# Performance work log

Measured on AMD Instinct MI355X. Metric: run time of the kernel, lower is better.

The kernel has to match this reference:

```python
import jax, jax.numpy as jnp
import numpy as np

N_NODES = 10000
N_GRAPHS = 64
NEG_SLOPE = 0.2  # PyG GATConv default


def _glorot(key, shape):
    fan_in, fan_out = shape[0], shape[-1]
    lim = jnp.sqrt(6.0 / (fan_in + fan_out))
    return jax.random.uniform(key, shape, jnp.float32, -lim, lim)


def setup_inputs() -> dict:
    key = jax.random.key(0)
    ks = jax.random.split(key, 12)
    x = jax.random.normal(ks[0], (N_NODES, 128), jnp.float32)
    edge_index = jax.random.randint(ks[1], (2, 160000), 0, N_NODES, jnp.int64)
    batch = jnp.sort(jax.random.randint(ks[2], (N_NODES,), 0, N_GRAPHS, jnp.int64))
    # GATConv 1: 128 -> 512 (heads=1)
    W1 = _glorot(ks[3], (128, 512))
    a_src1 = _glorot(ks[4], (1, 512))[0]
    a_dst1 = _glorot(ks[5], (1, 512))[0]
    b1 = jnp.zeros((512,), jnp.float32)
    # GATConv 2: 512 -> 64
    W2 = _glorot(ks[6], (512, 64))
    a_src2 = _glorot(ks[7], (1, 64))[0]
    a_dst2 = _glorot(ks[8], (1, 64))[0]
    b2 = jnp.zeros((64,), jnp.float32)
    # fc1: 64 -> 2
    fcW = _glorot(ks[9], (64, 2))
    fcb = jnp.zeros((2,), jnp.float32)
    return {"x": x, "edge_index": edge_index, "batch": batch,
            "W1": W1, "a_src1": a_src1, "a_dst1": a_dst1, "b1": b1,
            "W2": W2, "a_src2": a_src2, "a_dst2": a_dst2, "b2": b2,
            "fcW": fcW, "fcb": fcb}


def _gat_conv(x, src, dst, W, a_src, a_dst, b, n_nodes):
    # h: [N, out]; per-edge attention over incoming edges of each dst node
    h = x @ W
    alpha_s = h @ a_src  # [N]
    alpha_d = h @ a_dst  # [N]
    e = jax.nn.leaky_relu(alpha_s[src] + alpha_d[dst], NEG_SLOPE)  # [E]
    e_max = jax.ops.segment_max(e, dst, num_segments=n_nodes)
    ee = jnp.exp(e - e_max[dst])
    denom = jax.ops.segment_sum(ee, dst, num_segments=n_nodes)
    alpha = ee / denom[dst]  # softmax over edges sharing a dst
    out = jax.ops.segment_sum(alpha[:, None] * h[src], dst, num_segments=n_nodes)
    return out + b


def reference(x, edge_index, batch, W1, a_src1, a_dst1, b1,
              W2, a_src2, a_dst2, b2, fcW, fcb):
    n = x.shape[0]
    # add self loops (PyG GATConv default)
    loop = jnp.arange(n, dtype=edge_index.dtype)
    src = jnp.concatenate([edge_index[0], loop])
    dst = jnp.concatenate([edge_index[1], loop])
    h = jax.nn.relu(_gat_conv(x, src, dst, W1, a_src1, a_dst1, b1, n))
    h = jax.nn.relu(_gat_conv(h, src, dst, W2, a_src2, a_dst2, b2, n))
    # global mean pool over graphs
    sums = jax.ops.segment_sum(h, batch, num_segments=N_GRAPHS)
    cnts = jax.ops.segment_sum(jnp.ones((n,), h.dtype), batch, num_segments=N_GRAPHS)
    pooled = sums / jnp.maximum(cnts, 1.0)[:, None]
    # dropout is identity at inference
    return pooled @ fcW + fcb
```

## Files before the change

### kernel.cpp

```cpp
#include <hip/hip_runtime.h>
#include <hip/hip_bf16.h>

#define NEG_SLOPE 0.2f
#define CAP 64

typedef __attribute__((ext_vector_type(8))) short bf16x8;
typedef __attribute__((ext_vector_type(4))) float f32x4;

__device__ __forceinline__ unsigned short f2bf(float f){
  __hip_bfloat16 h = __float2bfloat16(f);
  return *reinterpret_cast<unsigned short*>(&h);
}

__global__ __launch_bounds__(256) void kPre(int N,
    const float* __restrict__ W1, const float* __restrict__ as1v, const float* __restrict__ ad1v,
    const float* __restrict__ W2, const float* __restrict__ as2v, const float* __restrict__ ad2v,
    float* __restrict__ ws1, float* __restrict__ wd1,
    float* __restrict__ ws2, float* __restrict__ wd2,
    unsigned short* __restrict__ W1T, unsigned short* __restrict__ W2T,
    int* __restrict__ cnt){
  const int t = threadIdx.x, blk = blockIdx.x, G = gridDim.x;
  __shared__ unsigned short tile[64][66];

  for (int i = blk * 256 + t; i < N; i += G * 256) cnt[i] = 0;

  if (blk < 160){
    int b = blk * 4 + (t >> 6);
    int l = t & 63;
    float s = 0.f, d = 0.f;
    if (b < 128){
      #pragma unroll
      for (int j = l; j < 512; j += 64){ float w = W1[b * 512 + j]; s += w * as1v[j]; d += w * ad1v[j]; }
    } else {
      int r = b - 128;
      float w = W2[r * 64 + l];
      s = w * as2v[l]; d = w * ad2v[l];
    }
    #pragma unroll
    for (int o = 32; o > 0; o >>= 1){ s += __shfl_xor(s, o); d += __shfl_xor(d, o); }
    if (l == 0){
      if (b < 128){ ws1[b] = s; wd1[b] = d; }
      else        { ws2[b - 128] = s; wd2[b - 128] = d; }
    }
  } else if (blk < 184){
    int u = blk - 160;
    int rr = t >> 6, cl = t & 63;
    if (u < 16){
      int kt = u >> 3, ct = u & 7;
      #pragma unroll
      for (int r = 0; r < 16; ++r){
        int kr = r * 4 + rr;
        tile[kr][cl] = f2bf(W1[(size_t)(kt * 64 + kr) * 512 + ct * 64 + cl]);
      }
      __syncthreads();
      #pragma unroll
      for (int r = 0; r < 16; ++r){
        int cr = r * 4 + rr;
        W1T[(size_t)(ct * 64 + cr) * 128 + kt * 64 + cl] = tile[cl][cr];
      }
    } else {
      int kt = u - 16;
      #pragma unroll
      for (int r = 0; r < 16; ++r){
        int kr = r * 4 + rr;
        tile[kr][cl] = f2bf(W2[(size_t)(kt * 64 + kr) * 64 + cl]);
      }
      __syncthreads();
      #pragma unroll
      for (int r = 0; r < 16; ++r){
        int cr = r * 4 + rr;
        W2T[(size_t)cr * 512 + kt * 64 + cl] = tile[cl][cr];
      }
    }
  }
}

__global__ __launch_bounds__(256) void kScat(const int* __restrict__ ei, int E, int N,
                                             int* __restrict__ cnt, int* __restrict__ csr,
                                             const float* __restrict__ x, const float* __restrict__ ws,
                                             const float* __restrict__ wd,
                                             float* __restrict__ as, float* __restrict__ ad,
                                             int nScat){
  int blk = blockIdx.x;
  if (blk < nScat){
    int i = blk * 256 + threadIdx.x;
    int Etot = E + N;
    if (i >= Etot) return;
    int s, d;
    if (i < E){ s = ei[i]; d = ei[E + i]; } else { s = i - E; d = i - E; }
    int p = atomicAdd(&cnt[d], 1);
    if (p < CAP) csr[(size_t)d * CAP + p] = s;
    return;
  }
  int n = (blk - nScat) * 4 + (threadIdx.x >> 6);
  if (n >= N) return;
  int l = threadIdx.x & 63;
  float2 xv = ((const float2*)(x + (size_t)n * 128))[l];
  float2 sv = ((const float2*)ws)[l];
  float2 dv = ((const float2*)wd)[l];
  float s = xv.x * sv.x + xv.y * sv.y;
  float d = xv.x * dv.x + xv.y * dv.y;
  #pragma unroll
  for (int o = 32; o > 0; o >>= 1){ s += __shfl_xor(s, o); d += __shfl_xor(d, o); }
  if (l == 0){ as[n] = s; ad[n] = d; }
}

template<int F, bool EPI>
__global__ __launch_bounds__(256) void k_aggw(const int* __restrict__ cnt, const int* __restrict__ csr,
    const float* __restrict__ as, const float* __restrict__ ad, const float* __restrict__ h,
    const float* __restrict__ bias, void* __restrict__ out, int N){
  int n = blockIdx.x * 4 + (threadIdx.x >> 6);
  if (n >= N) return;
  int l = threadIdx.x & 63;
  int deg = min(cnt[n], CAP);
  float adv = ad[n];
  int sr0 = 0; float v0 = -3.0e38f;
  if (l < deg){
    sr0 = csr[(size_t)n * CAP + l];
    float vv = as[sr0] + adv;
    v0 = (vv > 0.f) ? vv : NEG_SLOPE * vv;
  }
  float m = v0, ssum = (l < deg) ? 1.f : 0.f;
  #pragma unroll
  for (int o = 32; o > 0; o >>= 1){
    float m2 = __shfl_xor(m, o);
    float s2 = __shfl_xor(ssum, o);
    float mm = fmaxf(m, m2);
    float ns = 0.f;
    if (ssum > 0.f) ns += ssum * __expf(m - mm);
    if (s2  > 0.f) ns += s2  * __expf(m2 - mm);
    m = mm; ssum = ns;
  }
  float inv = 1.0f / ssum;
  float al0 = (l < deg) ? __expf(v0 - m) * inv : 0.f;

  constexpr int EPG = (F == 128) ? 2 : 4;
  constexpr int FL  = (F == 128) ? 32 : 16;
  int p = l / FL;
  int f = l % FL;
  float4 acc = make_float4(0.f, 0.f, 0.f, 0.f);
  int steps = (deg + EPG - 1) / EPG;
  #pragma unroll 4
  for (int i = 0; i < steps; ++i){
    int e = i * EPG + p;
    float a = __shfl(al0, e);
    int s  = __shfl(sr0, e);
    float4 hv = ((const float4*)(h + (size_t)s * F))[f];
    acc.x += a * hv.x; acc.y += a * hv.y; acc.z += a * hv.z; acc.w += a * hv.w;
  }
  if (F == 64){
    acc.x += __shfl_xor(acc.x, 16); acc.y += __shfl_xor(acc.y, 16);
    acc.z += __shfl_xor(acc.z, 16); acc.w += __shfl_xor(acc.w, 16);
  }
  acc.x += __shfl_xor(acc.x, 32); acc.y += __shfl_xor(acc.y, 32);
  acc.z += __shfl_xor(acc.z, 32); acc.w += __shfl_xor(acc.w, 32);
  if (l < FL){
    if (F == 128){
      unsigned short* ob = (unsigned short*)out;
      unsigned int p0 = (unsigned int)f2bf(acc.x) | ((unsigned int)f2bf(acc.y) << 16);
      unsigned int p1 = (unsigned int)f2bf(acc.z) | ((unsigned int)f2bf(acc.w) << 16);
      *(uint2*)(ob + (size_t)n * 128 + f * 4) = make_uint2(p0, p1);
    } else {
      float* ob = (float*)out;
      if (EPI){
        float4 bv = ((const float4*)bias)[f];
        acc.x = fmaxf(acc.x + bv.x, 0.f); acc.y = fmaxf(acc.y + bv.y, 0.f);
        acc.z = fmaxf(acc.z + bv.z, 0.f); acc.w = fmaxf(acc.w + bv.w, 0.f);
      }
      ((float4*)(ob + (size_t)n * F))[f] = acc;
    }
  }
}

#define LROWS 16
__global__ __launch_bounds__(256) void k_layer(
    const unsigned short* __restrict__ xab, const unsigned short* __restrict__ W1T,
    const float* __restrict__ b1,
    const unsigned short* __restrict__ W2T, const float* __restrict__ ws2,
    const float* __restrict__ wd2,
    float* __restrict__ h2, float* __restrict__ as2, float* __restrict__ ad2, int N){
  __shared__ __align__(16) unsigned short xs[16 * 136];
  __shared__ __align__(16) unsigned short gs[16 * 520];
  __shared__ float sred[4][16][2];
  int t = threadIdx.x;
  int w = t >> 6, l = t & 63;
  int lg = l >> 4, ln = l & 15;
  int n0 = blockIdx.x * LROWS;

  {
    int row = t >> 4, seg = t & 15;
    int n = n0 + row; if (n >= N) n = N - 1;
    *(int4*)&xs[row * 136 + seg * 8] = *(const int4*)&xab[(size_t)n * 128 + seg * 8];
  }
  __syncthreads();

  int c0 = w * 128;
  bf16x8 af[4];
  #pragma unroll
  for (int kt = 0; kt < 4; ++kt)
    af[kt] = *reinterpret_cast<const bf16x8*>(&xs[ln * 136 + kt * 32 + lg * 8]);

  f32x4 acc[8];
  #pragma unroll
  for (int nt = 0; nt < 8; ++nt) acc[nt] = (f32x4){0.f, 0.f, 0.f, 0.f};
  #pragma unroll
  for (int nt = 0; nt < 8; ++nt){
    const unsigned short* wp = W1T + (size_t)(c0 + nt * 16 + ln) * 128 + lg * 8;
    #pragma unroll
    for (int kt = 0; kt < 4; ++kt){
      bf16x8 bfr = *reinterpret_cast<const bf16x8*>(wp + kt * 32);
      acc[nt] = __builtin_amdgcn_mfma_f32_16x16x32_bf16(af[kt], bfr, acc[nt], 0, 0, 0);
    }
  }

  float ps4[4] = {0, 0, 0, 0}, pd4[4] = {0, 0, 0, 0};
  #pragma unroll
  for (int nt = 0; nt < 8; ++nt){
    int col = c0 + nt * 16 + ln;
    float bb = b1[col], wsv = ws2[col], wdv = wd2[col];
    #pragma unroll
    for (int r = 0; r < 4; ++r){
      float g = fmaxf(acc[nt][r] + bb, 0.f);
      gs[(lg * 4 + r) * 520 + col] = f2bf(g);
      ps4[r] += g * wsv;
      pd4[r] += g * wdv;
    }
  }
  #pragma unroll
  for (int o = 1; o < 16; o <<= 1){
    #pragma unroll
    for (int r = 0; r < 4; ++r){ ps4[r] += __shfl_xor(ps4[r], o); pd4[r] += __shfl_xor(pd4[r], o); }
  }
  if (ln == 0){
    #pragma unroll
    for (int r = 0; r < 4; ++r){ sred[w][lg * 4 + r][0] = ps4[r]; sred[w][lg * 4 + r][1] = pd4[r]; }
  }
  __syncthreads();
  if (t < 32){
    int r = t >> 1, c = t & 1;
    float v = sred[0][r][c] + sred[1][r][c] + sred[2][r][c] + sred[3][r][c];
    int n = n0 + r;
    if (n < N){ if (c == 0) as2[n] = v; else ad2[n] = v; }
  }

  f32x4 a0 = (f32x4){0.f, 0.f, 0.f, 0.f}, a1 = (f32x4){0.f, 0.f, 0.f, 0.f};
  const unsigned short* wp2 = W2T + (size_t)(w * 16 + ln) * 512 + lg * 8;
  #pragma unroll
  for (int kt = 0; kt < 16; kt += 2){
    bf16x8 afa = *reinterpret_cast<const bf16x8*>(&gs[ln * 520 + kt * 32 + lg * 8]);
    bf16x8 bfa = *reinterpret_cast<const bf16x8*>(wp2 + kt * 32);
    a0 = __builtin_amdgcn_mfma_f32_16x16x32_bf16(afa, bfa, a0, 0, 0, 0);
    bf16x8 afb = *reinterpret_cast<const bf16x8*>(&gs[ln * 520 + (kt + 1) * 32 + lg * 8]);
    bf16x8 bfb = *reinterpret_cast<const bf16x8*>(wp2 + (kt + 1) * 32);
    a1 = __builtin_amdgcn_mfma_f32_16x16x32_bf16(afb, bfb, a1, 0, 0, 0);
  }
  #pragma unroll
  for (int r = 0; r < 4; ++r){
    int n = n0 + lg * 4 + r;
    if (n < N) h2[(size_t)n * 64 + w * 16 + ln] = a0[r] + a1[r];
  }
}

__device__ __forceinline__ int lbound(const int* a, int n, int v){
  int lo = 0, hi = n;
  while (lo < hi){ int mid = (lo + hi) >> 1; if (a[mid] < v) lo = mid + 1; else hi = mid; }
  return lo;
}

__global__ __launch_bounds__(256) void k_poolfc(const float* __restrict__ g2, const int* __restrict__ batch,
                                                const float* __restrict__ fcW, const float* __restrict__ fcb,
                                                float* __restrict__ out, int N){
  int g = blockIdx.x;
  __shared__ int sb[2];
  if (threadIdx.x == 0){ sb[0] = lbound(batch, N, g); sb[1] = lbound(batch, N, g + 1); }
  __syncthreads();
  int r0 = sb[0], r1 = sb[1];
  int f = threadIdx.x & 63, ch = threadIdx.x >> 6;
  float s = 0.f;
  for (int r = r0 + ch; r < r1; r += 4) s += g2[(size_t)r * 64 + f];
  __shared__ float red[4][64];
  red[ch][f] = s;
  __syncthreads();
  if (ch == 0){
    float tot = red[0][f] + red[1][f] + red[2][f] + red[3][f];
    float c = fmaxf((float)(r1 - r0), 1.f);
    float p = tot / c;
    float o0 = p * fcW[f * 2 + 0];
    float o1 = p * fcW[f * 2 + 1];
    #pragma unroll
    for (int o = 32; o > 0; o >>= 1){ o0 += __shfl_xor(o0, o); o1 += __shfl_xor(o1, o); }
    if (f == 0){ out[g * 2 + 0] = o0 + fcb[0]; out[g * 2 + 1] = o1 + fcb[1]; }
  }
}

extern "C" void kernel_launch(void* const* d_in, const int* in_sizes, int n_in,
                              void* d_out, int out_size, void* d_ws, size_t ws_size,
                              hipStream_t stream){
  const float* x    = (const float*)d_in[0];
  const int* ei     = (const int*)d_in[1];
  const int* batch  = (const int*)d_in[2];
  const float* W1   = (const float*)d_in[3];
  const float* as1w = (const float*)d_in[4];
  const float* ad1w = (const float*)d_in[5];
  const float* b1   = (const float*)d_in[6];
  const float* W2   = (const float*)d_in[7];
  const float* as2w = (const float*)d_in[8];
  const float* ad2w = (const float*)d_in[9];
  const float* b2   = (const float*)d_in[10];
  const float* fcW  = (const float*)d_in[11];
  const float* fcb  = (const float*)d_in[12];
  float* out = (float*)d_out;

  const int N    = in_sizes[2];
  const int E    = in_sizes[1] / 2;
  const int NG   = out_size / 2;
  const int Etot = E + N;

  char* base = (char*)d_ws;
  size_t o = 0;
  auto take = [&](size_t bytes) -> char* {
    char* r = base + o;
    o = (o + bytes + 255) & ~(size_t)255;
    return r;
  };
  unsigned short* xa  = (unsigned short*)take((size_t)(N + 16) * 128 * 2);
  float* h2   = (float*)take((size_t)(N + 16) * 64 * 4);
  float* g2   = (float*)take((size_t)(N + 16) * 64 * 4);
  float* as1  = (float*)take((size_t)N * 4);
  float* ad1  = (float*)take((size_t)N * 4);
  float* as2  = (float*)take((size_t)N * 4);
  float* ad2  = (float*)take((size_t)N * 4);
  float* ws1  = (float*)take(128 * 4);
  float* wd1  = (float*)take(128 * 4);
  float* ws2  = (float*)take(512 * 4);
  float* wd2  = (float*)take(512 * 4);
  unsigned short* W1T = (unsigned short*)take((size_t)128 * 512 * 2);
  unsigned short* W2T = (unsigned short*)take((size_t)512 * 64 * 2);
  int*   cnt  = (int*)take((size_t)N * 4);
  int*   csr  = (int*)take((size_t)N * CAP * 4);

  kPre<<<184, 256, 0, stream>>>(N, W1, as1w, ad1w, W2, as2w, ad2w,
                                ws1, wd1, ws2, wd2, W1T, W2T, cnt);

  const int nScat = (Etot + 255) / 256;
  kScat<<<nScat + (N + 3) / 4, 256, 0, stream>>>(ei, E, N, cnt, csr, x, ws1, wd1, as1, ad1, nScat);

  k_aggw<128, false><<<(N + 3) / 4, 256, 0, stream>>>(cnt, csr, as1, ad1, x, b1, (void*)xa, N);
  k_layer<<<(N + LROWS - 1) / LROWS, 256, 0, stream>>>(xa, W1T, b1, W2T, ws2, wd2, h2, as2, ad2, N);
  k_aggw<64, true><<<(N + 3) / 4, 256, 0, stream>>>(cnt, csr, as2, ad2, h2, b2, (void*)g2, N);

  k_poolfc<<<NG, 256, 0, stream>>>(g2, batch, fcW, fcb, out, N);
}
```

Baseline: 82.55 us.

## Fuse layer-1 aggregation into MLP kernel and gather from bf16 copy of x

Layer-1 edge-softmax aggregation now runs inside the layer kernel: each block aggregates its 16 nodes directly into shared memory before the MFMA matmuls. This removes one launch and the global round-trip of the aggregated bf16 features. The gather now reads a bf16 copy of x, made in the prologue kernel, which halves the bytes fetched per neighbor. The costs are an extra conversion pass over x and fewer blocks (N/16 instead of N/4) running the latency-bound gather phase.

```diff
diff --git a/kernel.cpp b/kernel.cpp
--- a/kernel.cpp
+++ b/kernel.cpp
@@ -11,18 +11,31 @@
   __hip_bfloat16 h = __float2bfloat16(f);
   return *reinterpret_cast<unsigned short*>(&h);
 }
-
-__global__ __launch_bounds__(256) void kPre(int N,
+__device__ __forceinline__ float bf2f(unsigned short u){
+  return __uint_as_float(((unsigned int)u) << 16);
+}
+
+__global__ __launch_bounds__(256) void kPre(int N, const float* __restrict__ x,
     const float* __restrict__ W1, const float* __restrict__ as1v, const float* __restrict__ ad1v,
     const float* __restrict__ W2, const float* __restrict__ as2v, const float* __restrict__ ad2v,
     float* __restrict__ ws1, float* __restrict__ wd1,
     float* __restrict__ ws2, float* __restrict__ wd2,
     unsigned short* __restrict__ W1T, unsigned short* __restrict__ W2T,
-    int* __restrict__ cnt){
+    unsigned short* __restrict__ xbf, int* __restrict__ cnt){
   const int t = threadIdx.x, blk = blockIdx.x, G = gridDim.x;
   __shared__ unsigned short tile[64][66];
 
   for (int i = blk * 256 + t; i < N; i += G * 256) cnt[i] = 0;
+
+  {
+    int total = N * 32;
+    for (int i = blk * 256 + t; i < total; i += G * 256){
+      float4 v = ((const float4*)x)[i];
+      unsigned int q0 = (unsigned int)f2bf(v.x) | ((unsigned int)f2bf(v.y) << 16);
+      unsigned int q1 = (unsigned int)f2bf(v.z) | ((unsigned int)f2bf(v.w) << 16);
+      ((uint2*)xbf)[i] = make_uint2(q0, q1);
+    }
+  }
 
   if (blk < 160){
     int b = blk * 4 + (t >> 6);
@@ -105,10 +118,148 @@
   if (l == 0){ as[n] = s; ad[n] = d; }
 }
 
-template<int F, bool EPI>
-__global__ __launch_bounds__(256) void k_aggw(const int* __restrict__ cnt, const int* __restrict__ csr,
+#define LROWS 16
+__global__ __launch_bounds__(256) void kAggLayer(
+    const int* __restrict__ cnt, const int* __restrict__ csr,
+    const float* __restrict__ as1, const float* __restrict__ ad1,
+    const unsigned short* __restrict__ xbf,
+    const unsigned short* __restrict__ W1T, const float* __restrict__ b1,
+    const unsigned short* __restrict__ W2T, const float* __restrict__ ws2,
+    const float* __restrict__ wd2,
+    float* __restrict__ h2, float* __restrict__ as2, float* __restrict__ ad2, int N){
+  __shared__ __align__(16) unsigned short xs[16 * 136];
+  __shared__ __align__(16) unsigned short gs[16 * 520];
+  __shared__ float sred[4][16][2];
+  int t = threadIdx.x;
+  int w = t >> 6, l = t & 63;
+  int lg = l >> 4, ln = l & 15;
+  int n0 = blockIdx.x * LROWS;
+
+  int p = l >> 4;
+  int fg = l & 15;
+  #pragma unroll
+  for (int i = 0; i < 4; ++i){
+    int row = w * 4 + i;
+    int n = n0 + row;
+    float accv[8] = {0.f, 0.f, 0.f, 0.f, 0.f, 0.f, 0.f, 0.f};
+    if (n < N){
+      int deg = min(cnt[n], CAP);
+      float adv = ad1[n];
+      int sr0 = 0; float v0 = -3.0e38f;
+      if (l < deg){
+        sr0 = csr[(size_t)n * CAP + l];
+        float vv = as1[sr0] + adv;
+        v0 = (vv > 0.f) ? vv : NEG_SLOPE * vv;
+      }
+      float m = v0, ssum = (l < deg) ? 1.f : 0.f;
+      #pragma unroll
+      for (int o = 32; o > 0; o >>= 1){
+        float m2 = __shfl_xor(m, o);
+        float s2 = __shfl_xor(ssum, o);
+        float mm = fmaxf(m, m2);
+        float ns = 0.f;
+        if (ssum > 0.f) ns += ssum * __expf(m - mm);
+        if (s2  > 0.f) ns += s2  * __expf(m2 - mm);
+        m = mm; ssum = ns;
+      }
+      float inv = 1.0f / ssum;
+      float al0 = (l < deg) ? __expf(v0 - m) * inv : 0.f;
+      int steps = (deg + 3) >> 2;
+      for (int st = 0; st < steps; ++st){
+        int e = st * 4 + p;
+        float a = __shfl(al0, e);
+        int s  = __shfl(sr0, e);
+        int4 rv = *(const int4*)(xbf + (size_t)s * 128 + fg * 8);
+        const unsigned short* u = (const unsigned short*)&rv;
+        #pragma unroll
+        for (int j = 0; j < 8; ++j) accv[j] += a * bf2f(u[j]);
+      }
+      #pragma unroll
+      for (int j = 0; j < 8; ++j){
+        accv[j] += __shfl_xor(accv[j], 16);
+        accv[j] += __shfl_xor(accv[j], 32);
+      }
+    }
+    if (l < 16){
+      unsigned int q0 = (unsigned int)f2bf(accv[0]) | ((unsigned int)f2bf(accv[1]) << 16);
+      unsigned int q1 = (unsigned int)f2bf(accv[2]) | ((unsigned int)f2bf(accv[3]) << 16);
+      unsigned int q2 = (unsigned int)f2bf(accv[4]) | ((unsigned int)f2bf(accv[5]) << 16);
+      unsigned int q3 = (unsigned int)f2bf(accv[6]) | ((unsigned int)f2bf(accv[7]) << 16);
+      *(int4*)&xs[row * 136 + l * 8] = make_int4(q0, q1, q2, q3);
+    }
+  }
+  __syncthreads();
+
+  int c0 = w * 128;
+  bf16x8 af[4];
+  #pragma unroll
+  for (int kt = 0; kt < 4; ++kt)
+    af[kt] = *reinterpret_cast<const bf16x8*>(&xs[ln * 136 + kt * 32 + lg * 8]);
+
+  f32x4 acc[8];
+  #pragma unroll
+  for (int nt = 0; nt < 8; ++nt) acc[nt] = (f32x4){0.f, 0.f, 0.f, 0.f};
+  #pragma unroll
+  for (int nt = 0; nt < 8; ++nt){
+    const unsigned short* wp = W1T + (size_t)(c0 + nt * 16 + ln) * 128 + lg * 8;
+    #pragma unroll
+    for (int kt = 0; kt < 4; ++kt){
+      bf16x8 bfr = *reinterpret_cast<const bf16x8*>(wp + kt * 32);
+      acc[nt] = __builtin_amdgcn_mfma_f32_16x16x32_bf16(af[kt], bfr, acc[nt], 0, 0, 0);
+    }
+  }
+
+  float ps4[4] = {0, 0, 0, 0}, pd4[4] = {0, 0, 0, 0};
+  #pragma unroll
+  for (int nt = 0; nt < 8; ++nt){
+    int col = c0 + nt * 16 + ln;
+    float bb = b1[col], wsv = ws2[col], wdv = wd2[col];
+    #pragma unroll
+    for (int r = 0; r < 4; ++r){
+      float g = fmaxf(acc[nt][r] + bb, 0.f);
+      gs[(lg * 4 + r) * 520 + col] = f2bf(g);
+      ps4[r] += g * wsv;
+      pd4[r] += g * wdv;
+    }
+  }
+  #pragma unroll
+  for (int o = 1; o < 16; o <<= 1){
+    #pragma unroll
+    for (int r = 0; r < 4; ++r){ ps4[r] += __shfl_xor(ps4[r], o); pd4[r] += __shfl_xor(pd4[r], o); }
+  }
+  if (ln == 0){
+    #pragma unroll
+    for (int r = 0; r < 4; ++r){ sred[w][lg * 4 + r][0] = ps4[r]; sred[w][lg * 4 + r][1] = pd4[r]; }
+  }
+  __syncthreads();
+  if (t < 32){
+    int r = t >> 1, c = t & 1;
+    float v = sred[0][r][c] + sred[1][r][c] + sred[2][r][c] + sred[3][r][c];
+    int n = n0 + r;
+    if (n < N){ if (c == 0) as2[n] = v; else ad2[n] = v; }
+  }
+
+  f32x4 a0 = (f32x4){0.f, 0.f, 0.f, 0.f}, a1 = (f32x4){0.f, 0.f, 0.f, 0.f};
+  const unsigned short* wp2 = W2T + (size_t)(w * 16 + ln) * 512 + lg * 8;
+  #pragma unroll
+  for (int kt = 0; kt < 16; kt += 2){
+    bf16x8 afa = *reinterpret_cast<const bf16x8*>(&gs[ln * 520 + kt * 32 + lg * 8]);
+    bf16x8 bfa = *reinterpret_cast<const bf16x8*>(wp2 + kt * 32);
+    a0 = __builtin_amdgcn_mfma_f32_16x16x32_bf16(afa, bfa, a0, 0, 0, 0);
+    bf16x8 afb = *reinterpret_cast<const bf16x8*>(&gs[ln * 520 + (kt + 1) * 32 + lg * 8]);
+    bf16x8 bfb = *reinterpret_cast<const bf16x8*>(wp2 + (kt + 1) * 32);
+    a1 = __builtin_amdgcn_mfma_f32_16x16x32_bf16(afb, bfb, a1, 0, 0, 0);
+  }
+  #pragma unroll
+  for (int r = 0; r < 4; ++r){
+    int n = n0 + lg * 4 + r;
+    if (n < N) h2[(size_t)n * 64 + w * 16 + ln] = a0[r] + a1[r];
+  }
+}
+
+__global__ __launch_bounds__(256) void kAgg2(const int* __restrict__ cnt, const int* __restrict__ csr,
     const float* __restrict__ as, const float* __restrict__ ad, const float* __restrict__ h,
-    const float* __restrict__ bias, void* __restrict__ out, int N){
+    const float* __restrict__ bias, float* __restrict__ out, int N){
   int n = blockIdx.x * 4 + (threadIdx.x >> 6);
   if (n >= N) return;
   int l = threadIdx.x & 63;
@@ -134,130 +285,27 @@
   float inv = 1.0f / ssum;
   float al0 = (l < deg) ? __expf(v0 - m) * inv : 0.f;
 
-  constexpr int EPG = (F == 128) ? 2 : 4;
-  constexpr int FL  = (F == 128) ? 32 : 16;
-  int p = l / FL;
-  int f = l % FL;
+  int p = l >> 4;
+  int f = l & 15;
   float4 acc = make_float4(0.f, 0.f, 0.f, 0.f);
-  int steps = (deg + EPG - 1) / EPG;
+  int steps = (deg + 3) >> 2;
   #pragma unroll 4
   for (int i = 0; i < steps; ++i){
-    int e = i * EPG + p;
+    int e = i * 4 + p;
     float a = __shfl(al0, e);
     int s  = __shfl(sr0, e);
-    float4 hv = ((const float4*)(h + (size_t)s * F))[f];
+    float4 hv = ((const float4*)(h + (size_t)s * 64))[f];
     acc.x += a * hv.x; acc.y += a * hv.y; acc.z += a * hv.z; acc.w += a * hv.w;
   }
-  if (F == 64){
-    acc.x += __shfl_xor(acc.x, 16); acc.y += __shfl_xor(acc.y, 16);
-    acc.z += __shfl_xor(acc.z, 16); acc.w += __shfl_xor(acc.w, 16);
-  }
+  acc.x += __shfl_xor(acc.x, 16); acc.y += __shfl_xor(acc.y, 16);
+  acc.z += __shfl_xor(acc.z, 16); acc.w += __shfl_xor(acc.w, 16);
   acc.x += __shfl_xor(acc.x, 32); acc.y += __shfl_xor(acc.y, 32);
   acc.z += __shfl_xor(acc.z, 32); acc.w += __shfl_xor(acc.w, 32);
-  if (l < FL){
-    if (F == 128){
-      unsigned short* ob = (unsigned short*)out;
-      unsigned int p0 = (unsigned int)f2bf(acc.x) | ((unsigned int)f2bf(acc.y) << 16);
-      unsigned int p1 = (unsigned int)f2bf(acc.z) | ((unsigned int)f2bf(acc.w) << 16);
-      *(uint2*)(ob + (size_t)n * 128 + f * 4) = make_uint2(p0, p1);
-    } else {
-      float* ob = (float*)out;
-      if (EPI){
-        float4 bv = ((const float4*)bias)[f];
-        acc.x = fmaxf(acc.x + bv.x, 0.f); acc.y = fmaxf(acc.y + bv.y, 0.f);
-        acc.z = fmaxf(acc.z + bv.z, 0.f); acc.w = fmaxf(acc.w + bv.w, 0.f);
-      }
-      ((float4*)(ob + (size_t)n * F))[f] = acc;
-    }
-  }
-}
-
-#define LROWS 16
-__global__ __launch_bounds__(256) void k_layer(
-    const unsigned short* __restrict__ xab, const unsigned short* __restrict__ W1T,
-    const float* __restrict__ b1,
-    const unsigned short* __restrict__ W2T, const float* __restrict__ ws2,
-    const float* __restrict__ wd2,
-    float* __restrict__ h2, float* __restrict__ as2, float* __restrict__ ad2, int N){
-  __shared__ __align__(16) unsigned short xs[16 * 136];
-  __shared__ __align__(16) unsigned short gs[16 * 520];
-  __shared__ float sred[4][16][2];
-  int t = threadIdx.x;
-  int w = t >> 6, l = t & 63;
-  int lg = l >> 4, ln = l & 15;
-  int n0 = blockIdx.x * LROWS;
-
-  {
-    int row = t >> 4, seg = t & 15;
-    int n = n0 + row; if (n >= N) n = N - 1;
-    *(int4*)&xs[row * 136 + seg * 8] = *(const int4*)&xab[(size_t)n * 128 + seg * 8];
-  }
-  __syncthreads();
-
-  int c0 = w * 128;
-  bf16x8 af[4];
-  #pragma unroll
-  for (int kt = 0; kt < 4; ++kt)
-    af[kt] = *reinterpret_cast<const bf16x8*>(&xs[ln * 136 + kt * 32 + lg * 8]);
-
-  f32x4 acc[8];
-  #pragma unroll
-  for (int nt = 0; nt < 8; ++nt) acc[nt] = (f32x4){0.f, 0.f, 0.f, 0.f};
-  #pragma unroll
-  for (int nt = 0; nt < 8; ++nt){
-    const unsigned short* wp = W1T + (size_t)(c0 + nt * 16 + ln) * 128 + lg * 8;
-    #pragma unroll
-    for (int kt = 0; kt < 4; ++kt){
-      bf16x8 bfr = *reinterpret_cast<const bf16x8*>(wp + kt * 32);
-      acc[nt] = __builtin_amdgcn_mfma_f32_16x16x32_bf16(af[kt], bfr, acc[nt], 0, 0, 0);
-    }
-  }
-
-  float ps4[4] = {0, 0, 0, 0}, pd4[4] = {0, 0, 0, 0};
-  #pragma unroll
-  for (int nt = 0; nt < 8; ++nt){
-    int col = c0 + nt * 16 + ln;
-    float bb = b1[col], wsv = ws2[col], wdv = wd2[col];
-    #pragma unroll
-    for (int r = 0; r < 4; ++r){
-      float g = fmaxf(acc[nt][r] + bb, 0.f);
-      gs[(lg * 4 + r) * 520 + col] = f2bf(g);
-      ps4[r] += g * wsv;
-      pd4[r] += g * wdv;
-    }
-  }
-  #pragma unroll
-  for (int o = 1; o < 16; o <<= 1){
-    #pragma unroll
-    for (int r = 0; r < 4; ++r){ ps4[r] += __shfl_xor(ps4[r], o); pd4[r] += __shfl_xor(pd4[r], o); }
-  }
-  if (ln == 0){
-    #pragma unroll
-    for (int r = 0; r < 4; ++r){ sred[w][lg * 4 + r][0] = ps4[r]; sred[w][lg * 4 + r][1] = pd4[r]; }
-  }
-  __syncthreads();
-  if (t < 32){
-    int r = t >> 1, c = t & 1;
-    float v = sred[0][r][c] + sred[1][r][c] + sred[2][r][c] + sred[3][r][c];
-    int n = n0 + r;
-    if (n < N){ if (c == 0) as2[n] = v; else ad2[n] = v; }
-  }
-
-  f32x4 a0 = (f32x4){0.f, 0.f, 0.f, 0.f}, a1 = (f32x4){0.f, 0.f, 0.f, 0.f};
-  const unsigned short* wp2 = W2T + (size_t)(w * 16 + ln) * 512 + lg * 8;
-  #pragma unroll
-  for (int kt = 0; kt < 16; kt += 2){
-    bf16x8 afa = *reinterpret_cast<const bf16x8*>(&gs[ln * 520 + kt * 32 + lg * 8]);
-    bf16x8 bfa = *reinterpret_cast<const bf16x8*>(wp2 + kt * 32);
-    a0 = __builtin_amdgcn_mfma_f32_16x16x32_bf16(afa, bfa, a0, 0, 0, 0);
-    bf16x8 afb = *reinterpret_cast<const bf16x8*>(&gs[ln * 520 + (kt + 1) * 32 + lg * 8]);
-    bf16x8 bfb = *reinterpret_cast<const bf16x8*>(wp2 + (kt + 1) * 32);
-    a1 = __builtin_amdgcn_mfma_f32_16x16x32_bf16(afb, bfb, a1, 0, 0, 0);
-  }
-  #pragma unroll
-  for (int r = 0; r < 4; ++r){
-    int n = n0 + lg * 4 + r;
-    if (n < N) h2[(size_t)n * 64 + w * 16 + ln] = a0[r] + a1[r];
+  if (l < 16){
+    float4 bv = ((const float4*)bias)[f];
+    acc.x = fmaxf(acc.x + bv.x, 0.f); acc.y = fmaxf(acc.y + bv.y, 0.f);
+    acc.z = fmaxf(acc.z + bv.z, 0.f); acc.w = fmaxf(acc.w + bv.w, 0.f);
+    ((float4*)(out + (size_t)n * 64))[f] = acc;
   }
 }
 
@@ -323,7 +371,7 @@
     o = (o + bytes + 255) & ~(size_t)255;
     return r;
   };
-  unsigned short* xa  = (unsigned short*)take((size_t)(N + 16) * 128 * 2);
+  unsigned short* xbf = (unsigned short*)take((size_t)(N + 16) * 128 * 2);
   float* h2   = (float*)take((size_t)(N + 16) * 64 * 4);
   float* g2   = (float*)take((size_t)(N + 16) * 64 * 4);
   float* as1  = (float*)take((size_t)N * 4);
@@ -339,15 +387,15 @@
   int*   cnt  = (int*)take((size_t)N * 4);
   int*   csr  = (int*)take((size_t)N * CAP * 4);
 
-  kPre<<<184, 256, 0, stream>>>(N, W1, as1w, ad1w, W2, as2w, ad2w,
-                                ws1, wd1, ws2, wd2, W1T, W2T, cnt);
+  kPre<<<184, 256, 0, stream>>>(N, x, W1, as1w, ad1w, W2, as2w, ad2w,
+                                ws1, wd1, ws2, wd2, W1T, W2T, xbf, cnt);
 
   const int nScat = (Etot + 255) / 256;
   kScat<<<nScat + (N + 3) / 4, 256, 0, stream>>>(ei, E, N, cnt, csr, x, ws1, wd1, as1, ad1, nScat);
 
-  k_aggw<128, false><<<(N + 3) / 4, 256, 0, stream>>>(cnt, csr, as1, ad1, x, b1, (void*)xa, N);
-  k_layer<<<(N + LROWS - 1) / LROWS, 256, 0, stream>>>(xa, W1T, b1, W2T, ws2, wd2, h2, as2, ad2, N);
-  k_aggw<64, true><<<(N + 3) / 4, 256, 0, stream>>>(cnt, csr, as2, ad2, h2, b2, (void*)g2, N);
+  kAggLayer<<<(N + LROWS - 1) / LROWS, 256, 0, stream>>>(cnt, csr, as1, ad1, xbf,
+                                                         W1T, b1, W2T, ws2, wd2, h2, as2, ad2, N);
+  kAgg2<<<(N + 3) / 4, 256, 0, stream>>>(cnt, csr, as2, ad2, h2, b2, g2, N);
 
   k_poolfc<<<NG, 256, 0, stream>>>(g2, batch, fcW, fcb, out, N);
 }
```

Result: no change. 82.54 us (-0.0%).
